# Optimization experiments

Hardware: AMD Instinct MI355X
Metric: run time of the kernel (lower is better)

## Reference

```python
import jax, jax.numpy as jnp
import numpy as np

V, E, H, O = 32000, 300, 300, 9   # vocab, embed_dim, hidden, n_tags
B, T = 128, 512                   # batch, seq_len


def setup_inputs() -> dict:
    key = jax.random.key(0)
    ks = jax.random.split(key, 10)
    w = lambda k, shape: (jax.random.normal(k, shape, jnp.float32) * 0.05)
    return {
        "x": jax.random.randint(ks[0], (B, T), 0, V),
        "emb_table": w(ks[1], (V, E)),
        "W_ih_f": w(ks[2], (4 * H, E)),   # torch gate order: i, f, g, o
        "W_hh_f": w(ks[3], (4 * H, H)),
        "b_f": w(ks[4], (4 * H,)),        # b_ih + b_hh fused (mathematically identical)
        "W_ih_b": w(ks[5], (4 * H, E)),
        "W_hh_b": w(ks[6], (4 * H, H)),
        "b_b": w(ks[7], (4 * H,)),
        "W_lin": w(ks[8], (O, 2 * H)),
        "b_lin": w(ks[9], (O,)),
    }


def _lstm_dir(emb, W_ih, W_hh, b, reverse):
    # Pre-project inputs once (time-batched GEMM), scan only the recurrence.
    xp = jnp.einsum("bte,ge->btg", emb, W_ih) + b      # [B,T,4H]
    xp = jnp.swapaxes(xp, 0, 1)                         # [T,B,4H]
    Bv = emb.shape[0]
    Hv = W_hh.shape[1]
    z = jnp.zeros((Bv, Hv), emb.dtype)

    def step(carry, xt):
        h, c = carry
        gates = xt + h @ W_hh.T                          # [B,4H]
        i, f, g, o = jnp.split(gates, 4, axis=-1)
        c = jax.nn.sigmoid(f) * c + jax.nn.sigmoid(i) * jnp.tanh(g)
        h = jax.nn.sigmoid(o) * jnp.tanh(c)
        return (h, c), h

    _, hs = jax.lax.scan(step, (z, z), xp, reverse=reverse)
    return jnp.swapaxes(hs, 0, 1)                        # [B,T,H]


def reference(x, emb_table, W_ih_f, W_hh_f, b_f, W_ih_b, W_hh_b, b_b, W_lin, b_lin):
    emb = emb_table[x]                                   # [B,T,E]
    hf = _lstm_dir(emb, W_ih_f, W_hh_f, b_f, reverse=False)
    hb = _lstm_dir(emb, W_ih_b, W_hh_b, b_b, reverse=True)
    out = jnp.concatenate([hf, hb], axis=-1) @ W_lin.T + b_lin  # [B,T,O]
    return jax.nn.softmax(out, axis=-1)
```

## Files before the change

kernel.cpp:

```cpp
#include <hip/hip_runtime.h>
#include <stdint.h>

#define Tn 512
#define Bn 128
#define NTOK (Bn*Tn)
#define En 300
#define Hn 300
#define On 9
#define LDK 328
#define HS 60
#define NSL 5
#define NCH 8
#define MC 16
#define NG 240
#define GLD 244
#define NBLK (2*NCH*NSL)
#define NTHR 960

#define HXW 304
#define HXSLOT (Bn*HXW)
#define HXDIR (2*HXSLOT)

typedef short s4v __attribute__((ext_vector_type(4)));
typedef short s8v __attribute__((ext_vector_type(8)));
typedef float f4v __attribute__((ext_vector_type(4)));

__device__ unsigned short g_hcat[NTOK * 2 * Hn];
__device__ unsigned int   g_hx[2 * HXDIR];

__device__ inline float b2f(unsigned short u){ unsigned v = ((unsigned)u) << 16; float f; __builtin_memcpy(&f, &v, 4); return f; }
__device__ inline unsigned short f2b(float f){ unsigned u; __builtin_memcpy(&u, &f, 4); u = u + 0x7fffu + ((u >> 16) & 1u); return (unsigned short)(u >> 16); }
__device__ inline float sigf(float x){ return 1.f / (1.f + __expf(-x)); }
__device__ inline float tanh_f(float x){ return 2.f / (1.f + __expf(-2.f * x)) - 1.f; }

__device__ inline void bar_lgkm(){ asm volatile("s_waitcnt lgkmcnt(0)\n\ts_barrier" ::: "memory"); }

__global__ __launch_bounds__(256) void k_zero()
{
    const int i = blockIdx.x * 256 + threadIdx.x;
    const int stride = gridDim.x * 256;
    for (int j = i; j < 2 * HXDIR; j += stride) g_hx[j] = 0xFFFFu;
}

__global__ __launch_bounds__(NTHR, 4) void k_lstm(
    const int* __restrict__ x, const float* __restrict__ emb,
    const float* __restrict__ W_ih_f, const float* __restrict__ W_hh_f, const float* __restrict__ b_f,
    const float* __restrict__ W_ih_b, const float* __restrict__ W_hh_b, const float* __restrict__ b_b)
{
    const int bi    = blockIdx.x;
    const int dir   = bi / (NCH * NSL);
    const int rem   = bi % (NCH * NSL);
    const int chunk = rem / NSL;
    const int slice = rem % NSL;
    const int j0    = slice * HS;
    const int b0    = chunk * MC;

    const float* Wih  = dir ? W_ih_b : W_ih_f;
    const float* Whh  = dir ? W_hh_b : W_hh_f;
    const float* bias = dir ? b_b    : b_f;
    unsigned int* hxd = g_hx + dir * HXDIR;

    __shared__ __align__(16) unsigned short Aemb[2][MC * LDK];
    __shared__ __align__(16) unsigned short Hb[MC * LDK];
    __shared__ __align__(16) float Gsm[MC * GLD];

    const int tid  = threadIdx.x;
    const int lane = tid & 63;
    const int wid  = tid >> 6;
    const int n0   = wid * 16;
    const int kq   = (lane >> 4) * 8;

    const int nloc = n0 + (lane & 15);
    const int q    = nloc / HS;
    const int jjn  = nloc % HS;
    const int grow = q * Hn + j0 + jjn;
    s8v bih[10], bhh[10];
#pragma unroll
    for (int kc = 0; kc < 10; kc++) {
        int kb = kc * 32 + kq;
        s8v fi = {0,0,0,0,0,0,0,0}, fh = {0,0,0,0,0,0,0,0};
#pragma unroll
        for (int j = 0; j < 8; j++) {
            int k = kb + j;
            if (k < En) {
                fi[j] = (short)f2b(Wih[grow * En + k]);
                fh[j] = (short)f2b(Whh[grow * Hn + k]);
            }
        }
        bih[kc] = fi; bhh[kc] = fh;
    }

    const int ebl = tid / HS;
    const int ejj = tid % HS;
    const float bi_i = bias[0 * Hn + j0 + ejj];
    const float bi_f = bias[1 * Hn + j0 + ejj];
    const float bi_g = bias[2 * Hn + j0 + ejj];
    const float bi_o = bias[3 * Hn + j0 + ejj];
    float creg = 0.f;
    const bool pub = ((ejj & 1) == 0);

    int goffA[5], loffA[5];
#pragma unroll
    for (int j = 0; j < 5; j++) {
        int i = tid + j * NTHR;
        int r = i / Hn, c = i - r * Hn;
        goffA[j] = (b0 + r) * HXW + c;
        loffA[j] = r * LDK + c;
    }

    {
        const int t0 = dir ? (Tn - 1) : 0;
        for (int i = tid; i < MC * 80; i += NTHR) {
            int r = i / 80, c = i - r * 80;
            s4v v = {0, 0, 0, 0};
            if (c < 75) {
                int xi = x[(b0 + r) * Tn + t0];
                float4 f = *(const float4*)(emb + (size_t)xi * En + c * 4);
                v[0] = (short)f2b(f.x); v[1] = (short)f2b(f.y);
                v[2] = (short)f2b(f.z); v[3] = (short)f2b(f.w);
            }
            *(s4v*)&Aemb[0][r * LDK + c * 4] = v;
        }
        if (tid < MC * 20) {
            int r = tid / 20, c = 300 + (tid % 20);
            Hb[r * LDK + c] = 0;
        }
        __syncthreads();
    }

#pragma unroll 1
    for (int s = 0; s < Tn; s++) {
        const int t   = dir ? (Tn - 1 - s) : s;
        const int cur = s & 1, nxt = cur ^ 1;

        float4 pf[2];
        const bool do_pf = (s + 1 < Tn);
        if (do_pf) {
            const int tn1 = dir ? (Tn - 2 - s) : (s + 1);
#pragma unroll
            for (int k = 0; k < 2; k++) {
                int i = tid + k * NTHR;
                if (i < MC * 80) {
                    int r = i / 80, c = i - r * 80;
                    if (c < 75) {
                        int xi = x[(b0 + r) * Tn + tn1];
                        pf[k] = *(const float4*)(emb + (size_t)xi * En + c * 4);
                    }
                }
            }
        }

        f4v acc = {0.f, 0.f, 0.f, 0.f};
        {
            const unsigned short* abase = &Aemb[cur][(lane & 15) * LDK + kq];
#pragma unroll
            for (int kc = 0; kc < 10; kc++) {
                s8v a = *(const s8v*)(abase + kc * 32);
                acc = __builtin_amdgcn_mfma_f32_16x16x32_bf16(a, bih[kc], acc, 0, 0, 0);
            }
        }

        if (s) {
            const unsigned tgt = (unsigned)(s - 1);
            const unsigned int* hsrc = hxd + (s & 1) * HXSLOT;
            unsigned int pv[5];
            unsigned pend = 0x1fu;
            do {
#pragma unroll
                for (int j = 0; j < 5; j++)
                    if (pend & (1u << j))
                        pv[j] = __hip_atomic_load(hsrc + goffA[j],
                                                  __ATOMIC_RELAXED, __HIP_MEMORY_SCOPE_AGENT);
#pragma unroll
                for (int j = 0; j < 5; j++)
                    if ((pv[j] & 0xffffu) == tgt) pend &= ~(1u << j);
            } while (pend);
#pragma unroll
            for (int j = 0; j < 5; j++)
                Hb[loffA[j]] = (unsigned short)(pv[j] >> 16);

            bar_lgkm();

            {
                const unsigned short* abase = &Hb[(lane & 15) * LDK + kq];
#pragma unroll
                for (int kc = 0; kc < 10; kc++) {
                    s8v a = *(const s8v*)(abase + kc * 32);
                    acc = __builtin_amdgcn_mfma_f32_16x16x32_bf16(a, bhh[kc], acc, 0, 0, 0);
                }
            }
        }

        {
            int col   = n0 + (lane & 15);
            int rbase = (lane >> 4) * 4;
#pragma unroll
            for (int r2 = 0; r2 < 4; r2++) Gsm[(rbase + r2) * GLD + col] = acc[r2];
        }
        bar_lgkm();

        {
            float gi  = Gsm[ebl * GLD + 0 * HS + ejj] + bi_i;
            float gf  = Gsm[ebl * GLD + 1 * HS + ejj] + bi_f;
            float gg2 = Gsm[ebl * GLD + 2 * HS + ejj] + bi_g;
            float go  = Gsm[ebl * GLD + 3 * HS + ejj] + bi_o;
            float iv = sigf(gi), fv = sigf(gf), gv = tanh_f(gg2), ov = sigf(go);
            creg = fv * creg + iv * gv;
            float h = ov * tanh_f(creg);
            unsigned hb16 = (unsigned)f2b(h);

            __hip_atomic_store(hxd + ((s + 1) & 1) * HXSLOT + (b0 + ebl) * HXW + (j0 + ejj),
                               (hb16 << 16) | (unsigned)s,
                               __ATOMIC_RELAXED, __HIP_MEMORY_SCOPE_AGENT);

            float hn = __shfl_down(h, 1);
            if (pub) {
                unsigned pkt = hb16 | ((unsigned)f2b(hn) << 16);
                __hip_atomic_store((unsigned int*)g_hcat
                                       + (((size_t)((b0 + ebl) * Tn + t)) * (2 * Hn) + dir * Hn + j0 + ejj) / 2,
                                   pkt, __ATOMIC_RELAXED, __HIP_MEMORY_SCOPE_AGENT);
            }
        }

        if (do_pf) {
#pragma unroll
            for (int k = 0; k < 2; k++) {
                int i = tid + k * NTHR;
                if (i < MC * 80) {
                    int r = i / 80, c = i - r * 80;
                    s4v v = {0, 0, 0, 0};
                    if (c < 75) {
                        v[0] = (short)f2b(pf[k].x); v[1] = (short)f2b(pf[k].y);
                        v[2] = (short)f2b(pf[k].z); v[3] = (short)f2b(pf[k].w);
                    }
                    *(s4v*)&Aemb[nxt][r * LDK + c * 4] = v;
                }
            }
        }
        bar_lgkm();
    }
}

__global__ __launch_bounds__(256) void k_out(
    const float* __restrict__ W_lin, const float* __restrict__ b_lin, float* __restrict__ out)
{
    __shared__ float Wl[On * 2 * Hn];
    __shared__ float bl[On];
    const int tid = threadIdx.x;
    for (int i = tid; i < On * 2 * Hn; i += 256) Wl[i] = W_lin[i];
    if (tid < On) bl[tid] = b_lin[tid];
    __syncthreads();

    const int lane = tid & 63;
    const int w    = tid >> 6;
    const int wg   = blockIdx.x * 4 + w;
    for (int it = 0; it < 16; it++) {
        const int p = wg * 16 + it;
        const unsigned short* row = g_hcat + (size_t)p * (2 * Hn);
        float part[On];
#pragma unroll
        for (int o = 0; o < On; o++) part[o] = 0.f;
        for (int c = 0; c < 10; c++) {
            int k = lane + 64 * c;
            if (k < 2 * Hn) {
                float v = b2f(row[k]);
#pragma unroll
                for (int o = 0; o < On; o++) part[o] += v * Wl[o * (2 * Hn) + k];
            }
        }
#pragma unroll
        for (int off = 32; off >= 1; off >>= 1) {
#pragma unroll
            for (int o = 0; o < On; o++) part[o] += __shfl_xor(part[o], off, 64);
        }
        if (lane == 0) {
            float lg[On];
            float m = -1e30f;
#pragma unroll
            for (int o = 0; o < On; o++) { lg[o] = part[o] + bl[o]; m = fmaxf(m, lg[o]); }
            float ssum = 0.f;
#pragma unroll
            for (int o = 0; o < On; o++) { lg[o] = __expf(lg[o] - m); ssum += lg[o]; }
            float inv = 1.f / ssum;
#pragma unroll
            for (int o = 0; o < On; o++) out[(size_t)p * On + o] = lg[o] * inv;
        }
    }
}

extern "C" void kernel_launch(void* const* d_in, const int* in_sizes, int n_in,
                              void* d_out, int out_size, void* d_ws, size_t ws_size,
                              hipStream_t stream)
{
    (void)in_sizes; (void)n_in; (void)out_size; (void)d_ws; (void)ws_size;
    const int* x = (const int*)d_in[0];
    const float* emb   = (const float*)d_in[1];
    const float* Wih_f = (const float*)d_in[2];
    const float* Whh_f = (const float*)d_in[3];
    const float* bf    = (const float*)d_in[4];
    const float* Wih_b = (const float*)d_in[5];
    const float* Whh_b = (const float*)d_in[6];
    const float* bb    = (const float*)d_in[7];
    const float* Wlin  = (const float*)d_in[8];
    const float* blin  = (const float*)d_in[9];
    float* out = (float*)d_out;

    k_zero<<<128, 256, 0, stream>>>();

    void* args[] = {
        (void*)&x, (void*)&emb,
        (void*)&Wih_f, (void*)&Whh_f, (void*)&bf,
        (void*)&Wih_b, (void*)&Whh_b, (void*)&bb
    };
    hipLaunchCooperativeKernel((const void*)k_lstm, dim3(NBLK), dim3(NTHR), args, 0, stream);

    k_out<<<1024, 256, 0, stream>>>(Wlin, blin, out);
}
```

Measured before the change: 2.501 ms.

## Poll only remote h slices, write own slice locally, cache token ids in LDS

Each block now writes its own slice of the new hidden state straight into shared memory. The cross-block spin-poll then fetches only the other 240 columns, which cuts the polled words per thread from 5 to 4 and replaces the per-element pending mask with a single combined check. The poll is moved ahead of the embedding prefetch so the global emb loads no longer sit in front of the critical-path wait. Token ids for the block's rows are staged once into LDS, which removes a global load per step in the prefetch. The cost is 32KB of extra LDS and a reordered prefetch path.

```diff
diff --git a/kernel.cpp b/kernel.cpp
--- a/kernel.cpp
+++ b/kernel.cpp
@@ -12,7 +12,6 @@
 #define NSL 5
 #define NCH 8
 #define MC 16
-#define NG 240
 #define GLD 244
 #define NBLK (2*NCH*NSL)
 #define NTHR 960
@@ -63,6 +62,7 @@
     __shared__ __align__(16) unsigned short Aemb[2][MC * LDK];
     __shared__ __align__(16) unsigned short Hb[MC * LDK];
     __shared__ __align__(16) float Gsm[MC * GLD];
+    __shared__ int Xl[MC * Tn];
 
     const int tid  = threadIdx.x;
     const int lane = tid & 63;
@@ -99,11 +99,13 @@
     float creg = 0.f;
     const bool pub = ((ejj & 1) == 0);
 
-    int goffA[5], loffA[5];
-#pragma unroll
-    for (int j = 0; j < 5; j++) {
-        int i = tid + j * NTHR;
-        int r = i / Hn, c = i - r * Hn;
+    int goffA[4], loffA[4];
+#pragma unroll
+    for (int j = 0; j < 4; j++) {
+        int i  = tid + j * NTHR;
+        int r  = i / (4 * HS);
+        int c2 = i - r * (4 * HS);
+        int c  = (c2 < j0) ? c2 : (c2 + HS);
         goffA[j] = (b0 + r) * HXW + c;
         loffA[j] = r * LDK + c;
     }
@@ -121,6 +123,10 @@
             }
             *(s4v*)&Aemb[0][r * LDK + c * 4] = v;
         }
+        for (int i = tid; i < MC * Tn; i += NTHR) {
+            int r = i >> 9, tt = i & (Tn - 1);
+            Xl[i] = x[(b0 + r) * Tn + tt];
+        }
         if (tid < MC * 20) {
             int r = tid / 20, c = 300 + (tid % 20);
             Hb[r * LDK + c] = 0;
@@ -132,6 +138,34 @@
     for (int s = 0; s < Tn; s++) {
         const int t   = dir ? (Tn - 1 - s) : s;
         const int cur = s & 1, nxt = cur ^ 1;
+
+        f4v acc = {0.f, 0.f, 0.f, 0.f};
+        {
+            const unsigned short* abase = &Aemb[cur][(lane & 15) * LDK + kq];
+#pragma unroll
+            for (int kc = 0; kc < 10; kc++) {
+                s8v a = *(const s8v*)(abase + kc * 32);
+                acc = __builtin_amdgcn_mfma_f32_16x16x32_bf16(a, bih[kc], acc, 0, 0, 0);
+            }
+        }
+
+        if (s) {
+            const unsigned tgt = (unsigned)(s - 1);
+            const unsigned int* hsrc = hxd + (s & 1) * HXSLOT;
+            unsigned int pv0, pv1, pv2, pv3;
+            for (;;) {
+                pv0 = __hip_atomic_load(hsrc + goffA[0], __ATOMIC_RELAXED, __HIP_MEMORY_SCOPE_AGENT);
+                pv1 = __hip_atomic_load(hsrc + goffA[1], __ATOMIC_RELAXED, __HIP_MEMORY_SCOPE_AGENT);
+                pv2 = __hip_atomic_load(hsrc + goffA[2], __ATOMIC_RELAXED, __HIP_MEMORY_SCOPE_AGENT);
+                pv3 = __hip_atomic_load(hsrc + goffA[3], __ATOMIC_RELAXED, __HIP_MEMORY_SCOPE_AGENT);
+                unsigned bad = ((pv0 ^ tgt) | (pv1 ^ tgt) | (pv2 ^ tgt) | (pv3 ^ tgt)) & 0xffffu;
+                if (!bad) break;
+            }
+            Hb[loffA[0]] = (unsigned short)(pv0 >> 16);
+            Hb[loffA[1]] = (unsigned short)(pv1 >> 16);
+            Hb[loffA[2]] = (unsigned short)(pv2 >> 16);
+            Hb[loffA[3]] = (unsigned short)(pv3 >> 16);
+        }
 
         float4 pf[2];
         const bool do_pf = (s + 1 < Tn);
@@ -143,51 +177,21 @@
                 if (i < MC * 80) {
                     int r = i / 80, c = i - r * 80;
                     if (c < 75) {
-                        int xi = x[(b0 + r) * Tn + tn1];
+                        int xi = Xl[(r << 9) + tn1];
                         pf[k] = *(const float4*)(emb + (size_t)xi * En + c * 4);
                     }
                 }
             }
         }
 
-        f4v acc = {0.f, 0.f, 0.f, 0.f};
-        {
-            const unsigned short* abase = &Aemb[cur][(lane & 15) * LDK + kq];
+        if (s) {
+            bar_lgkm();
+
+            const unsigned short* abase = &Hb[(lane & 15) * LDK + kq];
 #pragma unroll
             for (int kc = 0; kc < 10; kc++) {
                 s8v a = *(const s8v*)(abase + kc * 32);
-                acc = __builtin_amdgcn_mfma_f32_16x16x32_bf16(a, bih[kc], acc, 0, 0, 0);
-            }
-        }
-
-        if (s) {
-            const unsigned tgt = (unsigned)(s - 1);
-            const unsigned int* hsrc = hxd + (s & 1) * HXSLOT;
-            unsigned int pv[5];
-            unsigned pend = 0x1fu;
-            do {
-#pragma unroll
-                for (int j = 0; j < 5; j++)
-                    if (pend & (1u << j))
-                        pv[j] = __hip_atomic_load(hsrc + goffA[j],
-                                                  __ATOMIC_RELAXED, __HIP_MEMORY_SCOPE_AGENT);
-#pragma unroll
-                for (int j = 0; j < 5; j++)
-                    if ((pv[j] & 0xffffu) == tgt) pend &= ~(1u << j);
-            } while (pend);
-#pragma unroll
-            for (int j = 0; j < 5; j++)
-                Hb[loffA[j]] = (unsigned short)(pv[j] >> 16);
-
-            bar_lgkm();
-
-            {
-                const unsigned short* abase = &Hb[(lane & 15) * LDK + kq];
-#pragma unroll
-                for (int kc = 0; kc < 10; kc++) {
-                    s8v a = *(const s8v*)(abase + kc * 32);
-                    acc = __builtin_amdgcn_mfma_f32_16x16x32_bf16(a, bhh[kc], acc, 0, 0, 0);
-                }
+                acc = __builtin_amdgcn_mfma_f32_16x16x32_bf16(a, bhh[kc], acc, 0, 0, 0);
             }
         }
 
@@ -208,6 +212,8 @@
             creg = fv * creg + iv * gv;
             float h = ov * tanh_f(creg);
             unsigned hb16 = (unsigned)f2b(h);
+
+            Hb[ebl * LDK + j0 + ejj] = (unsigned short)hb16;
 
             __hip_atomic_store(hxd + ((s + 1) & 1) * HXSLOT + (b0 + ebl) * HXW + (j0 + ejj),
                                (hb16 << 16) | (unsigned)s,
```

New measurement: 2.031 ms (median of 2 runs). 1.23x faster.
